# Kernel tuning notes

Hardware: AMD Instinct MI355X
Metric: run time of the kernel (lower is better)

The kernel has to match this reference:

```python
import jax, jax.numpy as jnp
import numpy as np
import math

B, S, E, H, F = 4, 1024, 768, 12, 3072
D = E // H

def _sierpinski_mask(n=1024):
    i = np.arange(n)
    # mask[i,j] = 1 if (i & j) == 0 else 0
    return ((i[:, None] & i[None, :]) == 0).astype(np.int32)

def setup_inputs() -> dict:
    key = jax.random.key(0)
    ks = jax.random.split(key, 20)
    p = lambda k, shp: jax.random.normal(k, shp, dtype=jnp.float32) * 0.02
    return {
        'x':  jax.random.normal(ks[0], (B, S, E), dtype=jnp.float32),
        'smask': jnp.asarray(_sierpinski_mask(S)),
        'Wq': p(ks[1], (E, E)), 'bq': jnp.zeros((E,), jnp.float32),
        'Wk': p(ks[2], (E, E)), 'bk': jnp.zeros((E,), jnp.float32),
        'Wv': p(ks[3], (E, E)), 'bv': jnp.zeros((E,), jnp.float32),
        'Wo': p(ks[4], (E, E)), 'bo': jnp.zeros((E,), jnp.float32),
        'W1': p(ks[5], (E, F)), 'b1': jnp.zeros((F,), jnp.float32),
        'W2': p(ks[6], (F, E)), 'b2': jnp.zeros((E,), jnp.float32),
        'g1': jnp.ones((E,), jnp.float32), 'be1': jnp.zeros((E,), jnp.float32),
        'g2': jnp.ones((E,), jnp.float32), 'be2': jnp.zeros((E,), jnp.float32),
    }

def _layernorm(x, g, b, eps=1e-5):
    mu = jnp.mean(x, axis=-1, keepdims=True)
    var = jnp.mean(jnp.square(x - mu), axis=-1, keepdims=True)
    return (x - mu) * jax.lax.rsqrt(var + eps) * g + b

def _forward(x, smask_f, Wq, bq, Wk, bk, Wv, bv, Wo, bo, W1, b1, W2, b2, g1, be1, g2, be2):
    b_, s_, _ = x.shape
    Q = (x @ Wq + bq).reshape(b_, s_, H, D)
    K = (x @ Wk + bk).reshape(b_, s_, H, D)
    V = (x @ Wv + bv).reshape(b_, s_, H, D)
    scores = jnp.einsum('bqhd,bkhd->bhqk', Q, K) / math.sqrt(D)
    scores = scores * smask_f  # multiplicative 0/1 Sierpinski mask BEFORE softmax
    attn = jax.nn.softmax(scores, axis=-1)
    attended = jnp.einsum('bhqk,bkhd->bqhd', attn, V).reshape(b_, s_, E)
    attended = attended @ Wo + bo
    x = _layernorm(x + attended, g1, be1)  # dropout is identity (eval)
    ff = jax.nn.gelu(x @ W1 + b1, approximate=False) @ W2 + b2
    return _layernorm(x + ff, g2, be2)

def reference(x, smask, Wq, bq, Wk, bk, Wv, bv, Wo, bo, W1, b1, W2, b2, g1, be1, g2, be2):
    smask_f = smask.astype(x.dtype)
    return _forward(x, smask_f, Wq, bq, Wk, bk, Wv, bv, Wo, bo, W1, b1, W2, b2, g1, be1, g2, be2)
```

## Files before the change

### kernel.cpp

```cpp
#include <hip/hip_runtime.h>
#include <hip/hip_bf16.h>

constexpr int Bn = 4, Sn = 1024, En = 768, Hn = 12, Fn = 3072, Dn = 64;
constexpr int Mn = Bn * Sn;

typedef __attribute__((ext_vector_type(8))) short bf16x8;
typedef __attribute__((ext_vector_type(4))) float f32x4;

__device__ __forceinline__ short f2bs(float f) {
  unsigned u = __builtin_bit_cast(unsigned, f);
  unsigned r = (u + 0x7fffu + ((u >> 16) & 1u)) >> 16;
  return (short)(r & 0xffffu);
}

__device__ __forceinline__ float bs2f(short s) {
  unsigned u = ((unsigned)(unsigned short)s) << 16;
  return __builtin_bit_cast(float, u);
}

__device__ __forceinline__ void gload16(const void* g, void* l) {
  __builtin_amdgcn_global_load_lds(
      (const __attribute__((address_space(1))) void*)g,
      (__attribute__((address_space(3))) void*)l, 16, 0, 0);
}

__global__ __launch_bounds__(256) void prep_all(
    const float* __restrict__ x, short* __restrict__ xb,
    const float* __restrict__ Wq, const float* __restrict__ Wk,
    const float* __restrict__ Wv, const float* __restrict__ Wo,
    const float* __restrict__ W1, const float* __restrict__ W2,
    short* __restrict__ wt_qkv, short* __restrict__ wt_o,
    short* __restrict__ wt_1, short* __restrict__ wt_2) {
  int blk = blockIdx.x;
  if (blk < 3072) {
    int i = (blk * 256 + threadIdx.x) * 4;
    float4 f = *(const float4*)(x + i);
    short4 o;
    o.x = f2bs(f.x); o.y = f2bs(f.y); o.z = f2bs(f.z); o.w = f2bs(f.w);
    *(short4*)(xb + i) = o;
    return;
  }
  blk -= 3072;
  const float* W; short* Wt; int K, N, nbx;
  if (blk < 576)       { W = Wq; Wt = wt_qkv;             K = 768;  N = 768;  nbx = 24; }
  else if (blk < 1152) { W = Wk; Wt = wt_qkv + 768 * 768; K = 768;  N = 768;  nbx = 24; blk -= 576; }
  else if (blk < 1728) { W = Wv; Wt = wt_qkv + 1536 * 768;K = 768;  N = 768;  nbx = 24; blk -= 1152; }
  else if (blk < 2304) { W = Wo; Wt = wt_o;               K = 768;  N = 768;  nbx = 24; blk -= 1728; }
  else if (blk < 4608) { W = W1; Wt = wt_1;               K = 768;  N = 3072; nbx = 96; blk -= 2304; }
  else                 { W = W2; Wt = wt_2;               K = 3072; N = 768;  nbx = 24; blk -= 4608; }
  int bx = (blk % nbx) * 32, by = (blk / nbx) * 32;
  __shared__ float t[32][33];
  int tx = threadIdx.x & 31, ty = threadIdx.x >> 5;
#pragma unroll
  for (int i = ty; i < 32; i += 8)
    t[i][tx] = W[(size_t)(by + i) * N + bx + tx];
  __syncthreads();
#pragma unroll
  for (int i = ty; i < 32; i += 8)
    Wt[(size_t)(bx + i) * K + by + tx] = f2bs(t[tx][i]);
}

__global__ __launch_bounds__(256) void vtile_sum(
    const short* __restrict__ Vt, float* __restrict__ Vtile) {
  int bh = blockIdx.x;
  int d = threadIdx.x & 63, g = threadIdx.x >> 6;
#pragma unroll
  for (int i = 0; i < 4; ++i) {
    int kt = g * 4 + i;
    float s = 0.f;
    const short* p = Vt + ((size_t)bh * Dn + d) * Sn + kt * 64;
#pragma unroll
    for (int c = 0; c < 8; ++c) {
      bf16x8 v = *(const bf16x8*)(p + c * 8);
#pragma unroll
      for (int e = 0; e < 8; ++e) s += bs2f(v[e]);
    }
    Vtile[((size_t)bh * 16 + kt) * 64 + d] = s;
  }
}

template <int BM, int BN, int MODE, int OCC, int DBUF>
__global__ __launch_bounds__(256, OCC) void gemm_bt(
    const short* __restrict__ A, const short* __restrict__ Bt,
    int M, int N, int K,
    float* __restrict__ Cf, short* __restrict__ Cb,
    const float* __restrict__ bias0, const float* __restrict__ bias1,
    const float* __restrict__ bias2,
    short* __restrict__ Qo, short* __restrict__ Ko, short* __restrict__ Vto) {
  constexpr int WM = BM / 2, WN = BN / 2;
  constexpr int MR = WM / 16, NR = WN / 16;
  constexpr int NB = DBUF + 1;
  __shared__ short Asm[NB][BM * 64];
  __shared__ short Bsm[NB][BN * 64];
  const int tid = threadIdx.x, wv = tid >> 6, ln = tid & 63;

  const int gx = gridDim.x;
  const int nwg = gx * gridDim.y;
  const int d = blockIdx.y * gx + blockIdx.x;
  const int l = (d & 7) * (nwg >> 3) + (d >> 3);
  const int m0 = (l / gx) * BM, n0 = (l % gx) * BN;

  const int wm = (wv >> 1) * WM, wn = (wv & 1) * WN;
  f32x4 acc[MR][NR] = {};

  auto stage = [&](int bi, int k0) {
#pragma unroll
    for (int p = 0; p < BM / 32; ++p) {
      int off = p * 4096 + wv * 1024 + ln * 16;
      int r = off >> 7, sl = (off >> 4) & 7, ss = sl ^ (r & 7);
      gload16(A + (size_t)(m0 + r) * K + k0 + ss * 8,
              (char*)Asm[bi] + p * 4096 + wv * 1024);
    }
#pragma unroll
    for (int p = 0; p < BN / 32; ++p) {
      int off = p * 4096 + wv * 1024 + ln * 16;
      int r = off >> 7, sl = (off >> 4) & 7, ss = sl ^ (r & 7);
      gload16(Bt + (size_t)(n0 + r) * K + k0 + ss * 8,
              (char*)Bsm[bi] + p * 4096 + wv * 1024);
    }
  };

  auto compute = [&](int bi) {
    bf16x8 av[2][MR], bv[2][NR];
#pragma unroll
    for (int kk = 0; kk < 2; ++kk) {
#pragma unroll
      for (int i = 0; i < MR; ++i) {
        int ra = wm + i * 16 + (ln & 15);
        int sa = (kk * 4 + (ln >> 4)) ^ (ra & 7);
        av[kk][i] = *(const bf16x8*)((const char*)Asm[bi] + ra * 128 + sa * 16);
      }
#pragma unroll
      for (int i = 0; i < NR; ++i) {
        int rb = wn + i * 16 + (ln & 15);
        int sb = (kk * 4 + (ln >> 4)) ^ (rb & 7);
        bv[kk][i] = *(const bf16x8*)((const char*)Bsm[bi] + rb * 128 + sb * 16);
      }
    }
#pragma unroll
    for (int kk = 0; kk < 2; ++kk)
#pragma unroll
      for (int mi = 0; mi < MR; ++mi)
#pragma unroll
        for (int ni = 0; ni < NR; ++ni)
          acc[mi][ni] = __builtin_amdgcn_mfma_f32_16x16x32_bf16(
              av[kk][mi], bv[kk][ni], acc[mi][ni], 0, 0, 0);
  };

  const int nt = K >> 6;
  if constexpr (DBUF) {
    stage(0, 0);
    int buf = 0;
    for (int t = 0; t < nt; ++t) {
      __syncthreads();
      if (t + 1 < nt) stage(buf ^ 1, (t + 1) * 64);
      compute(buf);
      buf ^= 1;
    }
  } else {
    for (int t = 0; t < nt; ++t) {
      stage(0, t * 64);
      __syncthreads();
      compute(0);
      __syncthreads();
    }
  }

#pragma unroll
  for (int mi = 0; mi < MR; ++mi)
#pragma unroll
    for (int ni = 0; ni < NR; ++ni)
#pragma unroll
      for (int j = 0; j < 4; ++j) {
        int row = m0 + wm + mi * 16 + (ln >> 4) * 4 + j;
        int col = n0 + wn + ni * 16 + (ln & 15);
        float v = acc[mi][ni][j];
        if constexpr (MODE == 0) {
          Cf[(size_t)row * N + col] = v;
        } else if constexpr (MODE == 1) {
          int part = col / 768;
          int nn = col - part * 768;
          int h = nn >> 6, dd = nn & 63;
          int b = row >> 10, s = row & 1023;
          size_t bh = (size_t)(b * Hn + h);
          float bias = (part == 0) ? bias0[nn] : (part == 1) ? bias1[nn] : bias2[nn];
          short o = f2bs(v + bias);
          if (part == 0)       Qo[(bh * Sn + s) * Dn + dd] = o;
          else if (part == 1)  Ko[(bh * Sn + s) * Dn + dd] = o;
          else                 Vto[(bh * Dn + dd) * Sn + s] = o;
        } else {
          float u = v + bias0[col];
          float gl = 0.5f * u * (1.0f + erff(u * 0.70710678118654752f));
          Cb[(size_t)row * N + col] = f2bs(gl);
        }
      }
}

__device__ const int qt_order[16] = {0, 1, 2, 4, 8, 3, 5, 6, 9, 10, 12, 7, 11, 13, 14, 15};

__global__ __launch_bounds__(256, 2) void attn_kernel(
    const short* __restrict__ Qb, const short* __restrict__ Kb,
    const short* __restrict__ Vt, const float* __restrict__ Vtile,
    short* __restrict__ att) {
  __shared__ short Ksm[2][64 * 64];
  __shared__ short Vsm[2][64 * 64];
  __shared__ short P_lds[4][16 * 64];
  const int tid = threadIdx.x, wv = tid >> 6, ln = tid & 63;
  const int bh = blockIdx.x;
  const int qt = qt_order[blockIdx.y];
  const int q0 = qt * 64 + wv * 16;
  const int b = bh / Hn, h = bh - b * Hn;
  const int notqt = (~qt) & 15;
  const int nv = 1 << __popc(notqt);

  const size_t qoff = ((size_t)bh * Sn + q0) * Dn;
  bf16x8 aq[2];
#pragma unroll
  for (int kk = 0; kk < 2; ++kk)
    aq[kk] = *(const bf16x8*)(Qb + qoff + (size_t)(ln & 15) * Dn + kk * 32 + (ln >> 4) * 8);

  f32x4 o_acc[4] = {};
  float l_run[4] = {0.f, 0.f, 0.f, 0.f};
  short* Pw = (short*)&P_lds[wv][0];

  auto stage = [&](int bufi, int kt) {
#pragma unroll
    for (int i = 0; i < 2; ++i) {
      int off = i * 4096 + wv * 1024 + ln * 16;
      int r = off >> 7, sl = (off >> 4) & 7, ss = sl ^ (r & 7);
      gload16(Kb + ((size_t)bh * Sn + (size_t)kt * 64 + r) * Dn + ss * 8,
              (char*)Ksm[bufi] + i * 4096 + wv * 1024);
      gload16(Vt + ((size_t)bh * Dn + r) * Sn + (size_t)kt * 64 + ss * 8,
              (char*)Vsm[bufi] + i * 4096 + wv * 1024);
    }
  };

  stage(0, 0);
  __syncthreads();
  int buf = 0, kt = 0;
  while (true) {
    const int ktn = ((kt | qt) + 1) & notqt;
    if (ktn) stage(buf ^ 1, ktn);

    f32x4 s_acc[4] = {};
#pragma unroll
    for (int kk = 0; kk < 2; ++kk)
#pragma unroll
      for (int ni = 0; ni < 4; ++ni) {
        int rb = ni * 16 + (ln & 15);
        int sb = (kk * 4 + (ln >> 4)) ^ (rb & 7);
        bf16x8 bk = *(const bf16x8*)((const char*)Ksm[buf] + rb * 128 + sb * 16);
        s_acc[ni] = __builtin_amdgcn_mfma_f32_16x16x32_bf16(aq[kk], bk, s_acc[ni], 0, 0, 0);
      }

#pragma unroll
    for (int ni = 0; ni < 4; ++ni)
#pragma unroll
      for (int j = 0; j < 4; ++j) {
        int q = q0 + (ln >> 4) * 4 + j;
        int k = kt * 64 + ni * 16 + (ln & 15);
        float p = ((q & k) == 0) ? __expf(s_acc[ni][j] * 0.125f) : 1.0f;
        l_run[j] += p;
        int prow = (ln >> 4) * 4 + j;
        int pcol = ni * 16 + (ln & 15);
        int sw = (pcol >> 3) ^ (prow & 7);
        Pw[prow * 64 + sw * 8 + (pcol & 7)] = f2bs(p);
      }

#pragma unroll
    for (int kk = 0; kk < 2; ++kk) {
      int prow = ln & 15;
      int swp = (kk * 4 + (ln >> 4)) ^ (prow & 7);
      bf16x8 ap = *(const bf16x8*)(Pw + prow * 64 + swp * 8);
#pragma unroll
      for (int di = 0; di < 4; ++di) {
        int rv = di * 16 + (ln & 15);
        int sv = (kk * 4 + (ln >> 4)) ^ (rv & 7);
        bf16x8 bv = *(const bf16x8*)((const char*)Vsm[buf] + rv * 128 + sv * 16);
        o_acc[di] = __builtin_amdgcn_mfma_f32_16x16x32_bf16(ap, bv, o_acc[di], 0, 0, 0);
      }
    }

    __syncthreads();
    buf ^= 1;
    if (!ktn) break;
    kt = ktn;
  }

  float vc[4] = {0.f, 0.f, 0.f, 0.f};
  for (int t = 0; t < 16; ++t)
    if (qt & t) {
#pragma unroll
      for (int di = 0; di < 4; ++di)
        vc[di] += Vtile[((size_t)bh * 16 + t) * 64 + di * 16 + (ln & 15)];
    }
  const float skip_l = 64.0f * (float)(16 - nv);
  float ltot[4];
#pragma unroll
  for (int j = 0; j < 4; ++j) {
    float l = l_run[j];
#pragma unroll
    for (int o = 1; o < 16; o <<= 1) l += __shfl_xor(l, o);
    ltot[j] = l + skip_l;
  }
#pragma unroll
  for (int di = 0; di < 4; ++di)
#pragma unroll
    for (int j = 0; j < 4; ++j) {
      int s = q0 + (ln >> 4) * 4 + j;
      int e = h * 64 + di * 16 + (ln & 15);
      att[((size_t)b * Sn + s) * En + e] = f2bs((o_acc[di][j] + vc[di]) / ltot[j]);
    }
}

__device__ __forceinline__ float block_reduce_sum(float v, float* sbuf) {
#pragma unroll
  for (int o = 32; o > 0; o >>= 1) v += __shfl_down(v, o);
  int wv = threadIdx.x >> 6, ln = threadIdx.x & 63;
  __syncthreads();
  if (ln == 0) sbuf[wv] = v;
  __syncthreads();
  return sbuf[0] + sbuf[1] + sbuf[2] + sbuf[3];
}

__global__ __launch_bounds__(256) void ln_kernel(
    const float* __restrict__ xr, const float* __restrict__ yr,
    const float* __restrict__ bias, const float* __restrict__ g,
    const float* __restrict__ be, float* __restrict__ outf,
    short* __restrict__ outb) {
  __shared__ float sbuf[4];
  int row = blockIdx.x, tid = threadIdx.x;
  size_t base = (size_t)row * En;
  float u[3];
  float s = 0.f;
#pragma unroll
  for (int t = 0; t < 3; ++t) {
    int i = tid + t * 256;
    u[t] = xr[base + i] + yr[base + i] + bias[i];
    s += u[t];
  }
  s = block_reduce_sum(s, sbuf);
  float mean = s * (1.0f / En);
  float s2 = 0.f;
#pragma unroll
  for (int t = 0; t < 3; ++t) { float d = u[t] - mean; s2 += d * d; }
  s2 = block_reduce_sum(s2, sbuf);
  float rstd = rsqrtf(s2 * (1.0f / En) + 1e-5f);
#pragma unroll
  for (int t = 0; t < 3; ++t) {
    int i = tid + t * 256;
    float o = (u[t] - mean) * rstd * g[i] + be[i];
    outf[base + i] = o;
    if (outb) outb[base + i] = f2bs(o);
  }
}

extern "C" void kernel_launch(void* const* d_in, const int* in_sizes, int n_in,
                              void* d_out, int out_size, void* d_ws, size_t ws_size,
                              hipStream_t stream) {
  const float* x   = (const float*)d_in[0];
  const float* Wq  = (const float*)d_in[2];
  const float* bq  = (const float*)d_in[3];
  const float* Wk  = (const float*)d_in[4];
  const float* bk  = (const float*)d_in[5];
  const float* Wv  = (const float*)d_in[6];
  const float* bv  = (const float*)d_in[7];
  const float* Wo  = (const float*)d_in[8];
  const float* bo  = (const float*)d_in[9];
  const float* W1  = (const float*)d_in[10];
  const float* b1  = (const float*)d_in[11];
  const float* W2  = (const float*)d_in[12];
  const float* b2  = (const float*)d_in[13];
  const float* g1  = (const float*)d_in[14];
  const float* be1 = (const float*)d_in[15];
  const float* g2  = (const float*)d_in[16];
  const float* be2 = (const float*)d_in[17];
  float* out = (float*)d_out;
  char* ws = (char*)d_ws;

  constexpr size_t OFF_XB    = 0;
  constexpr size_t OFF_WTQKV = 6291456;
  constexpr size_t OFF_VTILE = 6291456;
  constexpr size_t OFF_WTO   = 9830400;
  constexpr size_t OFF_Q     = 11010048;
  constexpr size_t OFF_K     = 17301504;
  constexpr size_t OFF_VT    = 23592960;
  constexpr size_t OFF_FF1   = 0;
  constexpr size_t OFF_WT1   = 29884416;
  constexpr size_t OFF_WT2   = 34603008;
  constexpr size_t OFF_Y     = 39321600;
  constexpr size_t OFF_X1    = 51904512;
  constexpr size_t OFF_X1B   = 64487424;

  short* xb     = (short*)(ws + OFF_XB);
  short* attb   = (short*)(ws + OFF_XB);
  short* wt_qkv = (short*)(ws + OFF_WTQKV);
  float* vtile  = (float*)(ws + OFF_VTILE);
  short* wt_o   = (short*)(ws + OFF_WTO);
  short* wt_1   = (short*)(ws + OFF_WT1);
  short* wt_2   = (short*)(ws + OFF_WT2);
  short* qb     = (short*)(ws + OFF_Q);
  short* kb     = (short*)(ws + OFF_K);
  short* vt     = (short*)(ws + OFF_VT);
  float* y1     = (float*)(ws + OFF_Y);
  float* y2     = (float*)(ws + OFF_Y);
  float* x1     = (float*)(ws + OFF_X1);
  short* x1b    = (short*)(ws + OFF_X1B);
  short* ff1    = (short*)(ws + OFF_FF1);

  prep_all<<<9984, 256, 0, stream>>>(x, xb, Wq, Wk, Wv, Wo, W1, W2,
                                     wt_qkv, wt_o, wt_1, wt_2);

  gemm_bt<128, 128, 1, 3, 0><<<dim3(18, 32), 256, 0, stream>>>(xb, wt_qkv, Mn, 2304, 768,
      nullptr, nullptr, bq, bk, bv, qb, kb, vt);
  vtile_sum<<<48, 256, 0, stream>>>(vt, vtile);
  attn_kernel<<<dim3(48, 16), 256, 0, stream>>>(qb, kb, vt, vtile, attb);
  gemm_bt<64, 64, 0, 4, 1><<<dim3(12, 64), 256, 0, stream>>>(attb, wt_o, Mn, 768, 768,
      y1, nullptr, nullptr, nullptr, nullptr, nullptr, nullptr, nullptr);
  ln_kernel<<<Mn, 256, 0, stream>>>(x, y1, bo, g1, be1, x1, x1b);
  gemm_bt<128, 128, 2, 3, 0><<<dim3(24, 32), 256, 0, stream>>>(x1b, wt_1, Mn, 3072, 768,
      nullptr, ff1, b1, nullptr, nullptr, nullptr, nullptr, nullptr);
  gemm_bt<64, 64, 0, 4, 1><<<dim3(12, 64), 256, 0, stream>>>(ff1, wt_2, Mn, 768, 3072,
      y2, nullptr, nullptr, nullptr, nullptr, nullptr, nullptr, nullptr);
  ln_kernel<<<Mn, 256, 0, stream>>>(x1, y2, b2, g2, be2, out, nullptr);
}
```

Baseline: 272.2 us.

## Single-buffer attention K/V staging and vectorize layernorm with 192 threads

The attention kernel drops double-buffered K/V shared-memory staging. Each tile is now loaded and synchronized before compute, which halves LDS use so more blocks can be resident, but it loses the overlap of the next tile's load with the current MFMA work. The layernorm kernel is rewritten to use 192 threads, each handling one float4. It does a single-pass reduction per statistic with fewer barriers and emits vectorized stores.

```diff
diff --git a/kernel.cpp b/kernel.cpp
--- a/kernel.cpp
+++ b/kernel.cpp
@@ -202,8 +202,8 @@
     const short* __restrict__ Qb, const short* __restrict__ Kb,
     const short* __restrict__ Vt, const float* __restrict__ Vtile,
     short* __restrict__ att) {
-  __shared__ short Ksm[2][64 * 64];
-  __shared__ short Vsm[2][64 * 64];
+  __shared__ short Ksm[64 * 64];
+  __shared__ short Vsm[64 * 64];
   __shared__ short P_lds[4][16 * 64];
   const int tid = threadIdx.x, wv = tid >> 6, ln = tid & 63;
   const int bh = blockIdx.x;
@@ -223,24 +223,22 @@
   float l_run[4] = {0.f, 0.f, 0.f, 0.f};
   short* Pw = (short*)&P_lds[wv][0];
 
-  auto stage = [&](int bufi, int kt) {
+  auto stage = [&](int kt) {
 #pragma unroll
     for (int i = 0; i < 2; ++i) {
       int off = i * 4096 + wv * 1024 + ln * 16;
       int r = off >> 7, sl = (off >> 4) & 7, ss = sl ^ (r & 7);
       gload16(Kb + ((size_t)bh * Sn + (size_t)kt * 64 + r) * Dn + ss * 8,
-              (char*)Ksm[bufi] + i * 4096 + wv * 1024);
+              (char*)Ksm + i * 4096 + wv * 1024);
       gload16(Vt + ((size_t)bh * Dn + r) * Sn + (size_t)kt * 64 + ss * 8,
-              (char*)Vsm[bufi] + i * 4096 + wv * 1024);
+              (char*)Vsm + i * 4096 + wv * 1024);
     }
   };
 
-  stage(0, 0);
-  __syncthreads();
-  int buf = 0, kt = 0;
+  int kt = 0;
   while (true) {
-    const int ktn = ((kt | qt) + 1) & notqt;
-    if (ktn) stage(buf ^ 1, ktn);
+    stage(kt);
+    __syncthreads();
 
     f32x4 s_acc[4] = {};
 #pragma unroll
@@ -249,7 +247,7 @@
       for (int ni = 0; ni < 4; ++ni) {
         int rb = ni * 16 + (ln & 15);
         int sb = (kk * 4 + (ln >> 4)) ^ (rb & 7);
-        bf16x8 bk = *(const bf16x8*)((const char*)Ksm[buf] + rb * 128 + sb * 16);
+        bf16x8 bk = *(const bf16x8*)((const char*)Ksm + rb * 128 + sb * 16);
         s_acc[ni] = __builtin_amdgcn_mfma_f32_16x16x32_bf16(aq[kk], bk, s_acc[ni], 0, 0, 0);
       }
 
@@ -276,13 +274,13 @@
       for (int di = 0; di < 4; ++di) {
         int rv = di * 16 + (ln & 15);
         int sv = (kk * 4 + (ln >> 4)) ^ (rv & 7);
-        bf16x8 bv = *(const bf16x8*)((const char*)Vsm[buf] + rv * 128 + sv * 16);
+        bf16x8 bv = *(const bf16x8*)((const char*)Vsm + rv * 128 + sv * 16);
         o_acc[di] = __builtin_amdgcn_mfma_f32_16x16x32_bf16(ap, bv, o_acc[di], 0, 0, 0);
       }
     }
 
+    const int ktn = ((kt | qt) + 1) & notqt;
     __syncthreads();
-    buf ^= 1;
     if (!ktn) break;
     kt = ktn;
   }
@@ -313,45 +311,51 @@
     }
 }
 
-__device__ __forceinline__ float block_reduce_sum(float v, float* sbuf) {
-#pragma unroll
-  for (int o = 32; o > 0; o >>= 1) v += __shfl_down(v, o);
-  int wv = threadIdx.x >> 6, ln = threadIdx.x & 63;
-  __syncthreads();
-  if (ln == 0) sbuf[wv] = v;
-  __syncthreads();
-  return sbuf[0] + sbuf[1] + sbuf[2] + sbuf[3];
-}
-
-__global__ __launch_bounds__(256) void ln_kernel(
+__global__ __launch_bounds__(192) void ln_kernel(
     const float* __restrict__ xr, const float* __restrict__ yr,
     const float* __restrict__ bias, const float* __restrict__ g,
     const float* __restrict__ be, float* __restrict__ outf,
     short* __restrict__ outb) {
-  __shared__ float sbuf[4];
-  int row = blockIdx.x, tid = threadIdx.x;
-  size_t base = (size_t)row * En;
-  float u[3];
-  float s = 0.f;
-#pragma unroll
-  for (int t = 0; t < 3; ++t) {
-    int i = tid + t * 256;
-    u[t] = xr[base + i] + yr[base + i] + bias[i];
-    s += u[t];
-  }
-  s = block_reduce_sum(s, sbuf);
-  float mean = s * (1.0f / En);
-  float s2 = 0.f;
-#pragma unroll
-  for (int t = 0; t < 3; ++t) { float d = u[t] - mean; s2 += d * d; }
-  s2 = block_reduce_sum(s2, sbuf);
-  float rstd = rsqrtf(s2 * (1.0f / En) + 1e-5f);
-#pragma unroll
-  for (int t = 0; t < 3; ++t) {
-    int i = tid + t * 256;
-    float o = (u[t] - mean) * rstd * g[i] + be[i];
-    outf[base + i] = o;
-    if (outb) outb[base + i] = f2bs(o);
+  __shared__ float sbuf[3];
+  const int row = blockIdx.x, tid = threadIdx.x;
+  const int wv = tid >> 6, lnn = tid & 63;
+  const size_t base = (size_t)row * En;
+  const int i4 = tid * 4;
+
+  float4 xv = *(const float4*)(xr + base + i4);
+  float4 yv = *(const float4*)(yr + base + i4);
+  float4 bv = *(const float4*)(bias + i4);
+  float4 u;
+  u.x = xv.x + yv.x + bv.x; u.y = xv.y + yv.y + bv.y;
+  u.z = xv.z + yv.z + bv.z; u.w = xv.w + yv.w + bv.w;
+
+  float s = u.x + u.y + u.z + u.w;
+#pragma unroll
+  for (int o = 32; o > 0; o >>= 1) s += __shfl_down(s, o);
+  if (lnn == 0) sbuf[wv] = s;
+  __syncthreads();
+  float mean = (sbuf[0] + sbuf[1] + sbuf[2]) * (1.0f / En);
+
+  float4 dv;
+  dv.x = u.x - mean; dv.y = u.y - mean; dv.z = u.z - mean; dv.w = u.w - mean;
+  float s2 = dv.x * dv.x + dv.y * dv.y + dv.z * dv.z + dv.w * dv.w;
+#pragma unroll
+  for (int o = 32; o > 0; o >>= 1) s2 += __shfl_down(s2, o);
+  __syncthreads();
+  if (lnn == 0) sbuf[wv] = s2;
+  __syncthreads();
+  float rstd = rsqrtf((sbuf[0] + sbuf[1] + sbuf[2]) * (1.0f / En) + 1e-5f);
+
+  float4 gv = *(const float4*)(g + i4);
+  float4 ev = *(const float4*)(be + i4);
+  float4 ov;
+  ov.x = dv.x * rstd * gv.x + ev.x; ov.y = dv.y * rstd * gv.y + ev.y;
+  ov.z = dv.z * rstd * gv.z + ev.z; ov.w = dv.w * rstd * gv.w + ev.w;
+  *(float4*)(outf + base + i4) = ov;
+  if (outb) {
+    short4 ob;
+    ob.x = f2bs(ov.x); ob.y = f2bs(ov.y); ob.z = f2bs(ov.z); ob.w = f2bs(ov.w);
+    *(short4*)(outb + base + i4) = ob;
   }
 }
 
@@ -417,10 +421,10 @@
   attn_kernel<<<dim3(48, 16), 256, 0, stream>>>(qb, kb, vt, vtile, attb);
   gemm_bt<64, 64, 0, 4, 1><<<dim3(12, 64), 256, 0, stream>>>(attb, wt_o, Mn, 768, 768,
       y1, nullptr, nullptr, nullptr, nullptr, nullptr, nullptr, nullptr);
-  ln_kernel<<<Mn, 256, 0, stream>>>(x, y1, bo, g1, be1, x1, x1b);
+  ln_kernel<<<Mn, 192, 0, stream>>>(x, y1, bo, g1, be1, x1, x1b);
   gemm_bt<128, 128, 2, 3, 0><<<dim3(24, 32), 256, 0, stream>>>(x1b, wt_1, Mn, 3072, 768,
       nullptr, ff1, b1, nullptr, nullptr, nullptr, nullptr, nullptr);
   gemm_bt<64, 64, 0, 4, 1><<<dim3(12, 64), 256, 0, stream>>>(ff1, wt_2, Mn, 768, 3072,
       y2, nullptr, nullptr, nullptr, nullptr, nullptr, nullptr, nullptr);
-  ln_kernel<<<Mn, 256, 0, stream>>>(x1, y2, b2, g2, be2, out, nullptr);
-}
+  ln_kernel<<<Mn, 192, 0, stream>>>(x1, y2, b2, g2, be2, out, nullptr);
+}
```

New measurement: 269.6 us. No clear change (-1.0%).
